# Kernel optimization log

Measured on AMD Instinct MI355X. Metric: run time of the kernel, lower is better.

Reference implementation:

```python
import jax, jax.numpy as jnp
import numpy as np

B, S, H, D = 4, 2048, 12, 64
HIDDEN = H * D  # 768
WINDOW = 64     # config.local_attention // 2
ROPE_THETA = 10000.0  # local_rope_theta for sliding layers


def rotate_half(x):
    d = x.shape[-1] // 2
    return jnp.concatenate([-x[..., d:], x[..., :d]], axis=-1)


def setup_inputs() -> dict:
    key = jax.random.key(0)
    k1, k2, k3 = jax.random.split(key, 3)
    hidden_states = jax.random.normal(k1, (B, S, HIDDEN), dtype=jnp.float32)
    # RoPE tables (HF style): inv_freq over half dims, duplicated
    inv_freq = 1.0 / (ROPE_THETA ** (jnp.arange(0, D, 2, dtype=jnp.float32) / D))  # [D/2]
    pos = jnp.arange(S, dtype=jnp.float32)
    freqs = pos[:, None] * inv_freq[None, :]          # [S, D/2]
    emb = jnp.concatenate([freqs, freqs], axis=-1)    # [S, D]
    cos = jnp.broadcast_to(jnp.cos(emb)[None], (B, S, D))
    sin = jnp.broadcast_to(jnp.sin(emb)[None], (B, S, D))
    # sliding-window additive mask [B,1,S,S]
    idx = jnp.arange(S)
    allowed = jnp.abs(idx[:, None] - idx[None, :]) <= WINDOW
    neg = jnp.finfo(jnp.float32).min
    attention_mask = jnp.broadcast_to(
        jnp.where(allowed, 0.0, neg)[None, None], (B, 1, S, S)
    ).astype(jnp.float32)
    std = 0.02
    Wqkv_w = jax.random.normal(k2, (3 * HIDDEN, HIDDEN), dtype=jnp.float32) * std
    Wo_w = jax.random.normal(k3, (HIDDEN, HIDDEN), dtype=jnp.float32) * std
    return {"hidden_states": hidden_states, "cos": cos, "sin": sin,
            "attention_mask": attention_mask, "Wqkv_w": Wqkv_w, "Wo_w": Wo_w}


def reference(hidden_states, cos, sin, attention_mask, Wqkv_w, Wo_w):
    b, s, _ = hidden_states.shape
    scaling = D ** -0.5
    qkv = hidden_states @ Wqkv_w.T                       # [B,S,3*HIDDEN]
    qkv = qkv.reshape(b, s, 3, H, D)
    q = jnp.transpose(qkv[:, :, 0], (0, 2, 1, 3))        # [B,H,S,D]
    k = jnp.transpose(qkv[:, :, 1], (0, 2, 1, 3))
    v = jnp.transpose(qkv[:, :, 2], (0, 2, 1, 3))
    # RoPE with float32 intermediates (inputs already fp32 here)
    c = cos[:, None].astype(jnp.float32)                 # [B,1,S,D]
    sn = sin[:, None].astype(jnp.float32)
    qf, kf = q.astype(jnp.float32), k.astype(jnp.float32)
    q = (qf * c + rotate_half(qf) * sn).astype(q.dtype)
    k = (kf * c + rotate_half(kf) * sn).astype(k.dtype)
    # SDPA with explicit additive mask
    scores = jnp.einsum('bhqd,bhkd->bhqk', q, k) * scaling + attention_mask
    attn = jax.nn.softmax(scores, axis=-1)
    out = jnp.einsum('bhqk,bhkd->bhqd', attn, v)         # [B,H,S,D]
    out = jnp.transpose(out, (0, 2, 1, 3)).reshape(b, s, HIDDEN)
    return out @ Wo_w.T
```

## Files before the change

kernel.cpp:

```cpp
#include <hip/hip_runtime.h>
#include <math.h>


typedef __attribute__((ext_vector_type(8))) short short8;
typedef __attribute__((ext_vector_type(4))) float floatx4;

constexpr int kB = 4;
constexpr int kS = 2048;
constexpr int kH = 12;
constexpr int kD = 64;
constexpr int kHidden = 768;
constexpr int kQKV = 3 * kHidden;

__device__ __forceinline__ unsigned short f2bf(float f) {
  union { float f; unsigned int u; } x; x.f = f;
  unsigned int r = (x.u + 0x7fffu + ((x.u >> 16) & 1u)) >> 16;
  return (unsigned short)r;
}

__global__ __launch_bounds__(256) void cvt_all(
    const float* __restrict__ h, const float* __restrict__ wqkv,
    const float* __restrict__ wo, unsigned short* __restrict__ hb,
    unsigned short* __restrict__ wqb, unsigned short* __restrict__ wob) {
  constexpr int n1 = kB * kS * kHidden / 4;
  constexpr int n2 = kQKV * kHidden / 4;
  constexpr int n3 = kHidden * kHidden / 4;
  int i = blockIdx.x * 256 + threadIdx.x;
  const float* src;
  unsigned short* dst;
  if (i < n1) {
    src = h; dst = hb;
  } else if (i < n1 + n2) {
    i -= n1; src = wqkv; dst = wqb;
  } else {
    i -= n1 + n2; if (i >= n3) return; src = wo; dst = wob;
  }
  const float4 v = ((const float4*)src)[i];
  ushort4 o;
  o.x = f2bf(v.x); o.y = f2bf(v.y); o.z = f2bf(v.z); o.w = f2bf(v.w);
  ((ushort4*)dst)[i] = o;
}

__device__ __forceinline__ void gload_lds16(const unsigned short* g, unsigned short* l) {
  __builtin_amdgcn_global_load_lds(
      (const __attribute__((address_space(1))) unsigned int*)g,
      (__attribute__((address_space(3))) unsigned int*)l, 16, 0, 0);
}

__global__ __launch_bounds__(512) void gemm_qkv(
    const unsigned short* __restrict__ A,
    const unsigned short* __restrict__ B,
    const float* __restrict__ cosp, const float* __restrict__ sinp,
    unsigned short* __restrict__ Qr, unsigned short* __restrict__ Kr,
    unsigned short* __restrict__ Vt) {
  constexpr int K = kHidden;
  constexpr int NP = 2 * (K / 64);
  __shared__ unsigned short SH[128 * 136];
  unsigned short* Ah0 = SH;
  unsigned short* Ah1 = SH + 4096;
  unsigned short* Bh0 = SH + 8192;
  unsigned short* Bh1 = SH + 12288;

  const int tid = threadIdx.x;
  const int lane = tid & 63;
  const int wave = tid >> 6;
  const int m0 = blockIdx.x * 128;
  const int n0 = blockIdx.y * 128;

  const int sc = wave * 64 + lane;
  const int srow = sc >> 2;
  const int sgc = ((sc & 3) ^ ((srow >> 1) & 3)) * 8;
  const int ldsOff = sc * 8;
  const unsigned short* gA0 = A + (size_t)(m0 + srow) * K + sgc;
  const unsigned short* gB0 = B + (size_t)(n0 + srow) * K + sgc;

  const int wm = wave >> 1, wn = wave & 1;
  const int mr = wm * 32 + (lane & 15);
  const int nr = wn * 64 + (lane & 15);
  const int kq = lane >> 4;

  int aOff[2], bOff[4];
#pragma unroll
  for (int i = 0; i < 2; i++) {
    const int r = mr + i * 16;
    aOff[i] = (r * 4 + (kq ^ ((r >> 1) & 3))) * 8;
  }
#pragma unroll
  for (int j = 0; j < 4; j++) {
    const int r = nr + j * 16;
    bOff[j] = (r * 4 + (kq ^ ((r >> 1) & 3))) * 8;
  }

  floatx4 acc[2][4];
#pragma unroll
  for (int i = 0; i < 2; i++)
#pragma unroll
    for (int j = 0; j < 4; j++) acc[i][j] = (floatx4)(0.f);

  gload_lds16(gA0, &Ah0[ldsOff]);
  gload_lds16(gB0, &Bh0[ldsOff]);

  for (int p = 0; p < NP; ++p) {
    if (p + 1 < NP) {
      const int kn = ((p + 1) >> 1) * 64 + ((p + 1) & 1) * 32;
      unsigned short* Ad = ((p + 1) & 1) ? Ah1 : Ah0;
      unsigned short* Bd = ((p + 1) & 1) ? Bh1 : Bh0;
      gload_lds16(gA0 + kn, &Ad[ldsOff]);
      gload_lds16(gB0 + kn, &Bd[ldsOff]);
      asm volatile("s_waitcnt vmcnt(2)" ::: "memory");
    } else {
      asm volatile("s_waitcnt vmcnt(0)" ::: "memory");
    }
    __builtin_amdgcn_s_barrier();
    __builtin_amdgcn_sched_barrier(0);
    const unsigned short* Asb = (p & 1) ? Ah1 : Ah0;
    const unsigned short* Bsb = (p & 1) ? Bh1 : Bh0;
    short8 af[2], bf[4];
#pragma unroll
    for (int i = 0; i < 2; i++) af[i] = *(const short8*)&Asb[aOff[i]];
#pragma unroll
    for (int j = 0; j < 4; j++) bf[j] = *(const short8*)&Bsb[bOff[j]];
#pragma unroll
    for (int i = 0; i < 2; i++)
#pragma unroll
      for (int j = 0; j < 4; j++)
        acc[i][j] = __builtin_amdgcn_mfma_f32_16x16x32_bf16(af[i], bf[j],
                                                            acc[i][j], 0, 0, 0);
    __builtin_amdgcn_sched_barrier(0);
    __builtin_amdgcn_s_barrier();
  }

  unsigned short (*Obuf)[136] = (unsigned short (*)[136])SH;

  const int region = n0 / kHidden;
  const int b = m0 >> 11, s0 = m0 & 2047;
  const int h0 = (n0 % kHidden) >> 6;
  const int rowL0 = wm * 32 + kq * 4;

  if (region == 2) {
#pragma unroll
    for (int i = 0; i < 2; i++)
#pragma unroll
      for (int r = 0; r < 4; r++) {
        const int rowL = rowL0 + i * 16 + r;
#pragma unroll
        for (int j = 0; j < 4; j++)
          Obuf[wn * 64 + j * 16 + (lane & 15)][rowL] = f2bf(acc[i][j][r]);
      }
    __syncthreads();
#pragma unroll
    for (int it = 0; it < 4; it++) {
      const int t = tid + it * 512;
      const int s8 = t & 15, rowc = t >> 4;
      const int hl = rowc >> 6, d = rowc & 63;
      *(short8*)(Vt + ((size_t)(b * kH + h0 + hl) * kD + d) * kS + s0 + s8 * 8) =
          *(const short8*)&Obuf[rowc][s8 * 8];
    }
  } else {
    unsigned short* dst = (region == 0) ? Qr : Kr;
    const float qscale = (region == 0) ? 0.125f : 1.f;
#pragma unroll
    for (int i = 0; i < 2; i++)
#pragma unroll
      for (int r = 0; r < 4; r++) {
        const int rowL = rowL0 + i * 16 + r;
        const int s = s0 + rowL;
        const float* cs = cosp + ((size_t)(b * kS + s)) * kD;
        const float* sns = sinp + ((size_t)(b * kS + s)) * kD;
#pragma unroll
        for (int jp = 0; jp < 2; jp++) {
          const int colL = wn * 64 + jp * 16 + (lane & 15);
          const int d = colL & 63;
          const float c = cs[d], sn = sns[d];
          const float xlo = acc[i][jp][r], xhi = acc[i][jp + 2][r];
          Obuf[rowL][colL]      = f2bf((xlo * c - xhi * sn) * qscale);
          Obuf[rowL][colL + 32] = f2bf((xhi * c + xlo * sn) * qscale);
        }
      }
    __syncthreads();
#pragma unroll
    for (int it = 0; it < 4; it++) {
      const int t = tid + it * 512;
      const int d8 = t & 7, sl = (t >> 3) & 127, hl = t >> 10;
      *(short8*)(dst + ((size_t)(b * kH + h0 + hl) * kS + s0 + sl) * kD + d8 * 8) =
          *(const short8*)&Obuf[sl][hl * 64 + d8 * 8];
    }
  }
}

__global__ __launch_bounds__(256) void gemm_bf16_nt(
    const unsigned short* __restrict__ A, const unsigned short* __restrict__ B,
    float* __restrict__ C, int M, int N, int K) {
  __shared__ unsigned short As[128 * 64];
  __shared__ unsigned short Bs[128 * 64];

  const int tid = threadIdx.x;
  const int lane = tid & 63;
  const int wave = tid >> 6;
  const int m0 = blockIdx.x * 128;
  const int n0 = blockIdx.y * 128;

  int ldsS[4];
  const unsigned short* gA[4];
  const unsigned short* gB[4];
#pragma unroll
  for (int t = 0; t < 4; t++) {
    const int ci = (wave * 4 + t) * 64 + lane;
    const int row = ci >> 3;
    const int c = (ci & 7) ^ (row & 7);
    ldsS[t] = ci * 8;
    gA[t] = A + (size_t)(m0 + row) * K + c * 8;
    gB[t] = B + (size_t)(n0 + row) * K + c * 8;
  }

  const int wm = wave >> 1, wn = wave & 1;
  const int mr = wm * 64 + (lane & 15);
  const int nr = wn * 64 + (lane & 15);
  const int kq = lane >> 4;

  floatx4 acc[4][4];
#pragma unroll
  for (int i = 0; i < 4; i++)
#pragma unroll
    for (int j = 0; j < 4; j++) acc[i][j] = (floatx4)(0.f);

  for (int k0 = 0; k0 < K; k0 += 64) {
    if (k0) __syncthreads();
#pragma unroll
    for (int t = 0; t < 4; t++) {
      gload_lds16(gA[t] + k0, &As[ldsS[t]]);
      gload_lds16(gB[t] + k0, &Bs[ldsS[t]]);
    }
    __syncthreads();
#pragma unroll
    for (int s = 0; s < 2; s++) {
      short8 af[4], bf[4];
#pragma unroll
      for (int i = 0; i < 4; i++) {
        af[i] = *(const short8*)&As[(mr + i * 16) * 64 + (((s * 4 + kq) ^ (mr & 7)) * 8)];
        bf[i] = *(const short8*)&Bs[(nr + i * 16) * 64 + (((s * 4 + kq) ^ (nr & 7)) * 8)];
      }
#pragma unroll
      for (int i = 0; i < 4; i++)
#pragma unroll
        for (int j = 0; j < 4; j++)
          acc[i][j] = __builtin_amdgcn_mfma_f32_16x16x32_bf16(af[i], bf[j],
                                                              acc[i][j], 0, 0, 0);
    }
  }

  const int crow = m0 + wm * 64 + kq * 4;
  const int ccol = n0 + wn * 64 + (lane & 15);
#pragma unroll
  for (int i = 0; i < 4; i++)
#pragma unroll
    for (int r = 0; r < 4; r++) {
      float* cp = C + (size_t)(crow + i * 16 + r) * N + ccol;
#pragma unroll
      for (int j = 0; j < 4; j++) cp[j * 16] = acc[i][j][r];
    }
}

constexpr int AQT = 32;

__global__ __launch_bounds__(256) void attn_v3(
    const unsigned short* __restrict__ Qr, const unsigned short* __restrict__ Kr,
    const unsigned short* __restrict__ Vt, unsigned short* __restrict__ out) {
  __shared__ unsigned short Pfrag[2][5][64][8];
  __shared__ float Ssum[2][AQT];

  const int tid = threadIdx.x;
  const int lane = tid & 63;
  const int wave = tid >> 6;
  const int quad = lane >> 4;
  const int l15 = lane & 15;
  const int qbase = blockIdx.x * AQT;
  const int h = blockIdx.y, b = blockIdx.z;
  const int bh = b * kH + h;
  const int kbase = qbase - 64;
  const int tq = wave >> 1;
  const int kh = wave & 1;

  short8 vf[2][5];
  {
    const unsigned short* vbase = Vt + (size_t)bh * kD * kS;
#pragma unroll
    for (int nt = 0; nt < 2; nt++) {
      const unsigned short* vrow = vbase + (size_t)(kh * 32 + nt * 16 + l15) * kS;
#pragma unroll
      for (int kk = 0; kk < 5; kk++) {
        int s0 = kbase + kk * 32 + quad * 8;
        s0 = min(max(s0, 0), kS - 8);
        vf[nt][kk] = *(const short8*)(vrow + s0);
      }
    }
  }

  const unsigned short* qsrc =
      Qr + ((size_t)bh * kS + qbase + tq * 16 + l15) * kD + quad * 8;
  const short8 a0 = *(const short8*)qsrc;
  const short8 a1 = *(const short8*)(qsrc + 32);

  floatx4 acc[5];
  const unsigned short* ksrc = Kr + (size_t)bh * kS * kD;
#pragma unroll
  for (int g = 0; g < 5; g++) {
    int row = kbase + (kh * 5 + g) * 16 + l15;
    row = min(max(row, 0), kS - 1);
    const unsigned short* kp = ksrc + (size_t)row * kD + quad * 8;
    const short8 b0 = *(const short8*)kp;
    const short8 b1 = *(const short8*)(kp + 32);
    floatx4 z = (floatx4)(0.f);
    z = __builtin_amdgcn_mfma_f32_16x16x32_bf16(a0, b0, z, 0, 0, 0);
    z = __builtin_amdgcn_mfma_f32_16x16x32_bf16(a1, b1, z, 0, 0, 0);
    acc[g] = z;
  }

#pragma unroll
  for (int r = 0; r < 4; r++) {
    const int q = tq * 16 + quad * 4 + r;
    float s = 0.f;
#pragma unroll
    for (int g = 0; g < 5; g++) {
      const int key = (kh * 5 + g) * 16 + l15;
      const int kg_ = kbase + key;
      const bool valid = (key >= q) && (key <= q + 128) && (kg_ >= 0) && (kg_ < kS);
      const float e = valid ? __expf(acc[g][r]) : 0.f;
      s += e;
      Pfrag[tq][key >> 5][((key >> 3) & 3) * 16 + quad * 4 + r][key & 7] = f2bf(e);
    }
#pragma unroll
    for (int off = 1; off < 16; off <<= 1) s += __shfl_xor(s, off, 64);
    if (l15 == 0) Ssum[kh][q] = s;
  }
  __syncthreads();

  floatx4 o0 = (floatx4)(0.f), o1 = (floatx4)(0.f);
#pragma unroll
  for (int kk = 0; kk < 5; kk++) {
    const short8 pa = *(const short8*)&Pfrag[tq][kk][lane][0];
    o0 = __builtin_amdgcn_mfma_f32_16x16x32_bf16(pa, vf[0][kk], o0, 0, 0, 0);
    o1 = __builtin_amdgcn_mfma_f32_16x16x32_bf16(pa, vf[1][kk], o1, 0, 0, 0);
  }

  __syncthreads();
  unsigned short (*Ob)[68] = (unsigned short (*)[68])Pfrag;
#pragma unroll
  for (int r = 0; r < 4; r++) {
    const int q = tq * 16 + quad * 4 + r;
    const float inv = 1.f / (Ssum[0][q] + Ssum[1][q]);
    Ob[q][kh * 32 + l15] = f2bf(o0[r] * inv);
    Ob[q][kh * 32 + 16 + l15] = f2bf(o1[r] * inv);
  }
  __syncthreads();
  {
    const int q = tid >> 3, d8 = tid & 7;
    *(short8*)(out + ((size_t)(b * kS + qbase + q)) * kHidden + h * kD + d8 * 8) =
        *(const short8*)&Ob[q][d8 * 8];
  }
}

extern "C" void kernel_launch(void* const* d_in, const int* in_sizes, int n_in,
                              void* d_out, int out_size, void* d_ws,
                              size_t ws_size, hipStream_t stream) {
  const float* hidden = (const float*)d_in[0];
  const float* cosp = (const float*)d_in[1];
  const float* sinp = (const float*)d_in[2];
  const float* wqkv = (const float*)d_in[4];
  const float* wo = (const float*)d_in[5];
  float* out = (float*)d_out;

  const int M = kB * kS;
  const size_t szH = (size_t)M * kHidden;

  unsigned short* hbf = (unsigned short*)d_ws;
  unsigned short* wqkvbf = hbf + szH;
  unsigned short* wobf = wqkvbf + (size_t)kQKV * kHidden;
  unsigned short* attnbf = wobf + (size_t)kHidden * kHidden;
  unsigned short* Qrb = attnbf + szH;
  unsigned short* Krb = Qrb + szH;
  unsigned short* Vtb = Krb + szH;

  const int ncvt = (M * kHidden + kQKV * kHidden + kHidden * kHidden) / 4;
  cvt_all<<<(ncvt + 255) / 256, 256, 0, stream>>>(hidden, wqkv, wo, hbf,
                                                  wqkvbf, wobf);

  dim3 g1(M / 128, kQKV / 128);
  gemm_qkv<<<g1, 512, 0, stream>>>(hbf, wqkvbf, cosp, sinp, Qrb, Krb, Vtb);

  dim3 ga(kS / AQT, kH, kB);
  attn_v3<<<ga, 256, 0, stream>>>(Qrb, Krb, Vtb, attnbf);

  dim3 g2(M / 128, kHidden / 128);
  gemm_bf16_nt<<<g2, 256, 0, stream>>>(attnbf, wobf, out, M, kHidden, kHidden);
}
```

Measured before the change: 214.7 us.

## Rebalance GEMM tiling: 4-wave QKV blocks, narrower output projection tiles

The QKV GEMM drops from 8 to 4 waves per block. Each wave now computes a 64x64 subtile with 16 accumulators instead of 32x64, which halves the LDS fragment reloads per MFMA. Each thread issues two async global-to-LDS loads per stage to keep the 128x128 tile filled. The output projection GEMM moves from 128x128 to 128x64 tiles, which doubles its grid to give more CU occupancy with a small N. The trade-off is fewer waves to hide latency in the QKV kernel and more A-tile reloads in the projection.

```diff
diff --git a/kernel.cpp b/kernel.cpp
--- a/kernel.cpp
+++ b/kernel.cpp
@@ -47,7 +47,7 @@
       (__attribute__((address_space(3))) unsigned int*)l, 16, 0, 0);
 }
 
-__global__ __launch_bounds__(512) void gemm_qkv(
+__global__ __launch_bounds__(256) void gemm_qkv(
     const unsigned short* __restrict__ A,
     const unsigned short* __restrict__ B,
     const float* __restrict__ cosp, const float* __restrict__ sinp,
@@ -64,50 +64,60 @@
   const int tid = threadIdx.x;
   const int lane = tid & 63;
   const int wave = tid >> 6;
+  const int l15 = lane & 15;
   const int m0 = blockIdx.x * 128;
   const int n0 = blockIdx.y * 128;
 
-  const int sc = wave * 64 + lane;
-  const int srow = sc >> 2;
-  const int sgc = ((sc & 3) ^ ((srow >> 1) & 3)) * 8;
-  const int ldsOff = sc * 8;
-  const unsigned short* gA0 = A + (size_t)(m0 + srow) * K + sgc;
-  const unsigned short* gB0 = B + (size_t)(n0 + srow) * K + sgc;
+  int ldsOff[2];
+  const unsigned short* gA0[2];
+  const unsigned short* gB0[2];
+#pragma unroll
+  for (int t = 0; t < 2; t++) {
+    const int sc = wave * 128 + t * 64 + lane;
+    const int srow = sc >> 2;
+    const int sgc = ((sc & 3) ^ ((srow >> 1) & 3)) * 8;
+    ldsOff[t] = sc * 8;
+    gA0[t] = A + (size_t)(m0 + srow) * K + sgc;
+    gB0[t] = B + (size_t)(n0 + srow) * K + sgc;
+  }
 
   const int wm = wave >> 1, wn = wave & 1;
-  const int mr = wm * 32 + (lane & 15);
-  const int nr = wn * 64 + (lane & 15);
+  const int mr = wm * 64 + l15;
+  const int nr = wn * 64 + l15;
   const int kq = lane >> 4;
 
-  int aOff[2], bOff[4];
-#pragma unroll
-  for (int i = 0; i < 2; i++) {
-    const int r = mr + i * 16;
-    aOff[i] = (r * 4 + (kq ^ ((r >> 1) & 3))) * 8;
-  }
-#pragma unroll
-  for (int j = 0; j < 4; j++) {
-    const int r = nr + j * 16;
-    bOff[j] = (r * 4 + (kq ^ ((r >> 1) & 3))) * 8;
-  }
-
-  floatx4 acc[2][4];
-#pragma unroll
-  for (int i = 0; i < 2; i++)
+  int aOff[4], bOff[4];
+#pragma unroll
+  for (int i = 0; i < 4; i++) {
+    const int ra = mr + i * 16;
+    aOff[i] = (ra * 4 + (kq ^ ((ra >> 1) & 3))) * 8;
+    const int rb = nr + i * 16;
+    bOff[i] = (rb * 4 + (kq ^ ((rb >> 1) & 3))) * 8;
+  }
+
+  floatx4 acc[4][4];
+#pragma unroll
+  for (int i = 0; i < 4; i++)
 #pragma unroll
     for (int j = 0; j < 4; j++) acc[i][j] = (floatx4)(0.f);
 
-  gload_lds16(gA0, &Ah0[ldsOff]);
-  gload_lds16(gB0, &Bh0[ldsOff]);
+#pragma unroll
+  for (int t = 0; t < 2; t++) {
+    gload_lds16(gA0[t], &Ah0[ldsOff[t]]);
+    gload_lds16(gB0[t], &Bh0[ldsOff[t]]);
+  }
 
   for (int p = 0; p < NP; ++p) {
     if (p + 1 < NP) {
-      const int kn = ((p + 1) >> 1) * 64 + ((p + 1) & 1) * 32;
+      const int kn = (p + 1) * 32;
       unsigned short* Ad = ((p + 1) & 1) ? Ah1 : Ah0;
       unsigned short* Bd = ((p + 1) & 1) ? Bh1 : Bh0;
-      gload_lds16(gA0 + kn, &Ad[ldsOff]);
-      gload_lds16(gB0 + kn, &Bd[ldsOff]);
-      asm volatile("s_waitcnt vmcnt(2)" ::: "memory");
+#pragma unroll
+      for (int t = 0; t < 2; t++) {
+        gload_lds16(gA0[t] + kn, &Ad[ldsOff[t]]);
+        gload_lds16(gB0[t] + kn, &Bd[ldsOff[t]]);
+      }
+      asm volatile("s_waitcnt vmcnt(4)" ::: "memory");
     } else {
       asm volatile("s_waitcnt vmcnt(0)" ::: "memory");
     }
@@ -115,13 +125,14 @@
     __builtin_amdgcn_sched_barrier(0);
     const unsigned short* Asb = (p & 1) ? Ah1 : Ah0;
     const unsigned short* Bsb = (p & 1) ? Bh1 : Bh0;
-    short8 af[2], bf[4];
-#pragma unroll
-    for (int i = 0; i < 2; i++) af[i] = *(const short8*)&Asb[aOff[i]];
-#pragma unroll
-    for (int j = 0; j < 4; j++) bf[j] = *(const short8*)&Bsb[bOff[j]];
-#pragma unroll
-    for (int i = 0; i < 2; i++)
+    short8 af[4], bf[4];
+#pragma unroll
+    for (int i = 0; i < 4; i++) {
+      af[i] = *(const short8*)&Asb[aOff[i]];
+      bf[i] = *(const short8*)&Bsb[bOff[i]];
+    }
+#pragma unroll
+    for (int i = 0; i < 4; i++)
 #pragma unroll
       for (int j = 0; j < 4; j++)
         acc[i][j] = __builtin_amdgcn_mfma_f32_16x16x32_bf16(af[i], bf[j],
@@ -135,22 +146,22 @@
   const int region = n0 / kHidden;
   const int b = m0 >> 11, s0 = m0 & 2047;
   const int h0 = (n0 % kHidden) >> 6;
-  const int rowL0 = wm * 32 + kq * 4;
+  const int rowL0 = wm * 64 + kq * 4;
 
   if (region == 2) {
 #pragma unroll
-    for (int i = 0; i < 2; i++)
+    for (int i = 0; i < 4; i++)
 #pragma unroll
       for (int r = 0; r < 4; r++) {
         const int rowL = rowL0 + i * 16 + r;
 #pragma unroll
         for (int j = 0; j < 4; j++)
-          Obuf[wn * 64 + j * 16 + (lane & 15)][rowL] = f2bf(acc[i][j][r]);
+          Obuf[wn * 64 + j * 16 + l15][rowL] = f2bf(acc[i][j][r]);
       }
     __syncthreads();
 #pragma unroll
-    for (int it = 0; it < 4; it++) {
-      const int t = tid + it * 512;
+    for (int it = 0; it < 8; it++) {
+      const int t = tid + it * 256;
       const int s8 = t & 15, rowc = t >> 4;
       const int hl = rowc >> 6, d = rowc & 63;
       *(short8*)(Vt + ((size_t)(b * kH + h0 + hl) * kD + d) * kS + s0 + s8 * 8) =
@@ -160,7 +171,7 @@
     unsigned short* dst = (region == 0) ? Qr : Kr;
     const float qscale = (region == 0) ? 0.125f : 1.f;
 #pragma unroll
-    for (int i = 0; i < 2; i++)
+    for (int i = 0; i < 4; i++)
 #pragma unroll
       for (int r = 0; r < 4; r++) {
         const int rowL = rowL0 + i * 16 + r;
@@ -169,7 +180,7 @@
         const float* sns = sinp + ((size_t)(b * kS + s)) * kD;
 #pragma unroll
         for (int jp = 0; jp < 2; jp++) {
-          const int colL = wn * 64 + jp * 16 + (lane & 15);
+          const int colL = wn * 64 + jp * 16 + l15;
           const int d = colL & 63;
           const float c = cs[d], sn = sns[d];
           const float xlo = acc[i][jp][r], xhi = acc[i][jp + 2][r];
@@ -179,8 +190,8 @@
       }
     __syncthreads();
 #pragma unroll
-    for (int it = 0; it < 4; it++) {
-      const int t = tid + it * 512;
+    for (int it = 0; it < 8; it++) {
+      const int t = tid + it * 256;
       const int d8 = t & 7, sl = (t >> 3) & 127, hl = t >> 10;
       *(short8*)(dst + ((size_t)(b * kH + h0 + hl) * kS + s0 + sl) * kD + d8 * 8) =
           *(const short8*)&Obuf[sl][hl * 64 + d8 * 8];
@@ -192,72 +203,81 @@
     const unsigned short* __restrict__ A, const unsigned short* __restrict__ B,
     float* __restrict__ C, int M, int N, int K) {
   __shared__ unsigned short As[128 * 64];
-  __shared__ unsigned short Bs[128 * 64];
+  __shared__ unsigned short Bs[64 * 64];
 
   const int tid = threadIdx.x;
   const int lane = tid & 63;
   const int wave = tid >> 6;
+  const int l15 = lane & 15;
   const int m0 = blockIdx.x * 128;
-  const int n0 = blockIdx.y * 128;
-
-  int ldsS[4];
+  const int n0 = blockIdx.y * 64;
+
+  int ldsA[4];
   const unsigned short* gA[4];
-  const unsigned short* gB[4];
 #pragma unroll
   for (int t = 0; t < 4; t++) {
     const int ci = (wave * 4 + t) * 64 + lane;
     const int row = ci >> 3;
     const int c = (ci & 7) ^ (row & 7);
-    ldsS[t] = ci * 8;
+    ldsA[t] = ci * 8;
     gA[t] = A + (size_t)(m0 + row) * K + c * 8;
+  }
+  int ldsB[2];
+  const unsigned short* gB[2];
+#pragma unroll
+  for (int t = 0; t < 2; t++) {
+    const int ci = (wave * 2 + t) * 64 + lane;
+    const int row = ci >> 3;
+    const int c = (ci & 7) ^ (row & 7);
+    ldsB[t] = ci * 8;
     gB[t] = B + (size_t)(n0 + row) * K + c * 8;
   }
 
   const int wm = wave >> 1, wn = wave & 1;
-  const int mr = wm * 64 + (lane & 15);
-  const int nr = wn * 64 + (lane & 15);
+  const int mr = wm * 64 + l15;
+  const int nr = wn * 32 + l15;
   const int kq = lane >> 4;
 
-  floatx4 acc[4][4];
+  floatx4 acc[4][2];
 #pragma unroll
   for (int i = 0; i < 4; i++)
 #pragma unroll
-    for (int j = 0; j < 4; j++) acc[i][j] = (floatx4)(0.f);
+    for (int j = 0; j < 2; j++) acc[i][j] = (floatx4)(0.f);
 
   for (int k0 = 0; k0 < K; k0 += 64) {
     if (k0) __syncthreads();
 #pragma unroll
-    for (int t = 0; t < 4; t++) {
-      gload_lds16(gA[t] + k0, &As[ldsS[t]]);
-      gload_lds16(gB[t] + k0, &Bs[ldsS[t]]);
-    }
+    for (int t = 0; t < 4; t++) gload_lds16(gA[t] + k0, &As[ldsA[t]]);
+#pragma unroll
+    for (int t = 0; t < 2; t++) gload_lds16(gB[t] + k0, &Bs[ldsB[t]]);
     __syncthreads();
 #pragma unroll
     for (int s = 0; s < 2; s++) {
-      short8 af[4], bf[4];
-#pragma unroll
-      for (int i = 0; i < 4; i++) {
-        af[i] = *(const short8*)&As[(mr + i * 16) * 64 + (((s * 4 + kq) ^ (mr & 7)) * 8)];
-        bf[i] = *(const short8*)&Bs[(nr + i * 16) * 64 + (((s * 4 + kq) ^ (nr & 7)) * 8)];
-      }
+      short8 af[4], bf[2];
 #pragma unroll
       for (int i = 0; i < 4; i++)
-#pragma unroll
-        for (int j = 0; j < 4; j++)
+        af[i] = *(const short8*)&As[(mr + i * 16) * 64 + (((s * 4 + kq) ^ ((mr + i * 16) & 7)) * 8)];
+#pragma unroll
+      for (int j = 0; j < 2; j++)
+        bf[j] = *(const short8*)&Bs[(nr + j * 16) * 64 + (((s * 4 + kq) ^ ((nr + j * 16) & 7)) * 8)];
+#pragma unroll
+      for (int i = 0; i < 4; i++)
+#pragma unroll
+        for (int j = 0; j < 2; j++)
           acc[i][j] = __builtin_amdgcn_mfma_f32_16x16x32_bf16(af[i], bf[j],
                                                               acc[i][j], 0, 0, 0);
     }
   }
 
   const int crow = m0 + wm * 64 + kq * 4;
-  const int ccol = n0 + wn * 64 + (lane & 15);
+  const int ccol = n0 + wn * 32 + l15;
 #pragma unroll
   for (int i = 0; i < 4; i++)
 #pragma unroll
     for (int r = 0; r < 4; r++) {
       float* cp = C + (size_t)(crow + i * 16 + r) * N + ccol;
 #pragma unroll
-      for (int j = 0; j < 4; j++) cp[j * 16] = acc[i][j][r];
+      for (int j = 0; j < 2; j++) cp[j * 16] = acc[i][j][r];
     }
 }
 
@@ -386,11 +406,11 @@
                                                   wqkvbf, wobf);
 
   dim3 g1(M / 128, kQKV / 128);
-  gemm_qkv<<<g1, 512, 0, stream>>>(hbf, wqkvbf, cosp, sinp, Qrb, Krb, Vtb);
+  gemm_qkv<<<g1, 256, 0, stream>>>(hbf, wqkvbf, cosp, sinp, Qrb, Krb, Vtb);
 
   dim3 ga(kS / AQT, kH, kB);
   attn_v3<<<ga, 256, 0, stream>>>(Qrb, Krb, Vtb, attnbf);
 
-  dim3 g2(M / 128, kHidden / 128);
+  dim3 g2(M / 128, kHidden / 64);
   gemm_bf16_nt<<<g2, 256, 0, stream>>>(attnbf, wobf, out, M, kHidden, kHidden);
 }
```

Result: no change. 214.7 us (+0.0%).

## Widen attention query tile to 64 and halve output GEMM N-tile

Applied to the files above, without the earlier changes.

The attention kernel now handles 64 queries per block instead of 32. Each wave computes two 16-query subtiles against six key groups, so K and V fragment loads are reused across more queries and redundant window loads drop. The output projection GEMM uses 128x64 tiles, which doubles the grid from 384 to 768 blocks so the 256 CUs are better filled. In exchange each attention block uses more registers and LDS, and the GEMM tiles have lower arithmetic intensity.

```diff
diff --git a/kernel.cpp b/kernel.cpp
--- a/kernel.cpp
+++ b/kernel.cpp
@@ -192,81 +192,90 @@
     const unsigned short* __restrict__ A, const unsigned short* __restrict__ B,
     float* __restrict__ C, int M, int N, int K) {
   __shared__ unsigned short As[128 * 64];
-  __shared__ unsigned short Bs[128 * 64];
+  __shared__ unsigned short Bs[64 * 64];
 
   const int tid = threadIdx.x;
   const int lane = tid & 63;
   const int wave = tid >> 6;
+  const int l15 = lane & 15;
   const int m0 = blockIdx.x * 128;
-  const int n0 = blockIdx.y * 128;
-
-  int ldsS[4];
+  const int n0 = blockIdx.y * 64;
+
+  int ldsA[4];
   const unsigned short* gA[4];
-  const unsigned short* gB[4];
 #pragma unroll
   for (int t = 0; t < 4; t++) {
     const int ci = (wave * 4 + t) * 64 + lane;
     const int row = ci >> 3;
     const int c = (ci & 7) ^ (row & 7);
-    ldsS[t] = ci * 8;
+    ldsA[t] = ci * 8;
     gA[t] = A + (size_t)(m0 + row) * K + c * 8;
+  }
+  int ldsB[2];
+  const unsigned short* gB[2];
+#pragma unroll
+  for (int t = 0; t < 2; t++) {
+    const int ci = (wave * 2 + t) * 64 + lane;
+    const int row = ci >> 3;
+    const int c = (ci & 7) ^ (row & 7);
+    ldsB[t] = ci * 8;
     gB[t] = B + (size_t)(n0 + row) * K + c * 8;
   }
 
   const int wm = wave >> 1, wn = wave & 1;
-  const int mr = wm * 64 + (lane & 15);
-  const int nr = wn * 64 + (lane & 15);
+  const int mr = wm * 64 + l15;
+  const int nr = wn * 32 + l15;
   const int kq = lane >> 4;
 
-  floatx4 acc[4][4];
+  floatx4 acc[4][2];
 #pragma unroll
   for (int i = 0; i < 4; i++)
 #pragma unroll
-    for (int j = 0; j < 4; j++) acc[i][j] = (floatx4)(0.f);
+    for (int j = 0; j < 2; j++) acc[i][j] = (floatx4)(0.f);
 
   for (int k0 = 0; k0 < K; k0 += 64) {
     if (k0) __syncthreads();
 #pragma unroll
-    for (int t = 0; t < 4; t++) {
-      gload_lds16(gA[t] + k0, &As[ldsS[t]]);
-      gload_lds16(gB[t] + k0, &Bs[ldsS[t]]);
-    }
+    for (int t = 0; t < 4; t++) gload_lds16(gA[t] + k0, &As[ldsA[t]]);
+#pragma unroll
+    for (int t = 0; t < 2; t++) gload_lds16(gB[t] + k0, &Bs[ldsB[t]]);
     __syncthreads();
 #pragma unroll
     for (int s = 0; s < 2; s++) {
-      short8 af[4], bf[4];
-#pragma unroll
-      for (int i = 0; i < 4; i++) {
-        af[i] = *(const short8*)&As[(mr + i * 16) * 64 + (((s * 4 + kq) ^ (mr & 7)) * 8)];
-        bf[i] = *(const short8*)&Bs[(nr + i * 16) * 64 + (((s * 4 + kq) ^ (nr & 7)) * 8)];
-      }
+      short8 af[4], bf[2];
 #pragma unroll
       for (int i = 0; i < 4; i++)
-#pragma unroll
-        for (int j = 0; j < 4; j++)
+        af[i] = *(const short8*)&As[(mr + i * 16) * 64 + (((s * 4 + kq) ^ ((mr + i * 16) & 7)) * 8)];
+#pragma unroll
+      for (int j = 0; j < 2; j++)
+        bf[j] = *(const short8*)&Bs[(nr + j * 16) * 64 + (((s * 4 + kq) ^ ((nr + j * 16) & 7)) * 8)];
+#pragma unroll
+      for (int i = 0; i < 4; i++)
+#pragma unroll
+        for (int j = 0; j < 2; j++)
           acc[i][j] = __builtin_amdgcn_mfma_f32_16x16x32_bf16(af[i], bf[j],
                                                               acc[i][j], 0, 0, 0);
     }
   }
 
   const int crow = m0 + wm * 64 + kq * 4;
-  const int ccol = n0 + wn * 64 + (lane & 15);
+  const int ccol = n0 + wn * 32 + l15;
 #pragma unroll
   for (int i = 0; i < 4; i++)
 #pragma unroll
     for (int r = 0; r < 4; r++) {
       float* cp = C + (size_t)(crow + i * 16 + r) * N + ccol;
 #pragma unroll
-      for (int j = 0; j < 4; j++) cp[j * 16] = acc[i][j][r];
-    }
-}
-
-constexpr int AQT = 32;
-
-__global__ __launch_bounds__(256) void attn_v3(
+      for (int j = 0; j < 2; j++) cp[j * 16] = acc[i][j][r];
+    }
+}
+
+constexpr int AQT = 64;
+
+__global__ __launch_bounds__(256) void attn_v4(
     const unsigned short* __restrict__ Qr, const unsigned short* __restrict__ Kr,
     const unsigned short* __restrict__ Vt, unsigned short* __restrict__ out) {
-  __shared__ unsigned short Pfrag[2][5][64][8];
+  __shared__ unsigned short Pfrag[4][6][64][8];
   __shared__ float Ssum[2][AQT];
 
   const int tid = threadIdx.x;
@@ -281,14 +290,41 @@
   const int tq = wave >> 1;
   const int kh = wave & 1;
 
-  short8 vf[2][5];
+  short8 a0[2], a1[2];
+#pragma unroll
+  for (int qs = 0; qs < 2; qs++) {
+    const unsigned short* qsrc =
+        Qr + ((size_t)bh * kS + qbase + tq * 32 + qs * 16 + l15) * kD + quad * 8;
+    a0[qs] = *(const short8*)qsrc;
+    a1[qs] = *(const short8*)(qsrc + 32);
+  }
+
+  floatx4 acc[2][6];
+  const unsigned short* ksrc = Kr + (size_t)bh * kS * kD;
+#pragma unroll
+  for (int g = 0; g < 6; g++) {
+    int row = kbase + (kh * 6 + g) * 16 + l15;
+    row = min(max(row, 0), kS - 1);
+    const unsigned short* kp = ksrc + (size_t)row * kD + quad * 8;
+    const short8 b0 = *(const short8*)kp;
+    const short8 b1 = *(const short8*)(kp + 32);
+#pragma unroll
+    for (int qs = 0; qs < 2; qs++) {
+      floatx4 z = (floatx4)(0.f);
+      z = __builtin_amdgcn_mfma_f32_16x16x32_bf16(a0[qs], b0, z, 0, 0, 0);
+      z = __builtin_amdgcn_mfma_f32_16x16x32_bf16(a1[qs], b1, z, 0, 0, 0);
+      acc[qs][g] = z;
+    }
+  }
+
+  short8 vf[2][6];
   {
     const unsigned short* vbase = Vt + (size_t)bh * kD * kS;
 #pragma unroll
     for (int nt = 0; nt < 2; nt++) {
       const unsigned short* vrow = vbase + (size_t)(kh * 32 + nt * 16 + l15) * kS;
 #pragma unroll
-      for (int kk = 0; kk < 5; kk++) {
+      for (int kk = 0; kk < 6; kk++) {
         int s0 = kbase + kk * 32 + quad * 8;
         s0 = min(max(s0, 0), kS - 8);
         vf[nt][kk] = *(const short8*)(vrow + s0);
@@ -296,65 +332,60 @@
     }
   }
 
-  const unsigned short* qsrc =
-      Qr + ((size_t)bh * kS + qbase + tq * 16 + l15) * kD + quad * 8;
-  const short8 a0 = *(const short8*)qsrc;
-  const short8 a1 = *(const short8*)(qsrc + 32);
-
-  floatx4 acc[5];
-  const unsigned short* ksrc = Kr + (size_t)bh * kS * kD;
-#pragma unroll
-  for (int g = 0; g < 5; g++) {
-    int row = kbase + (kh * 5 + g) * 16 + l15;
-    row = min(max(row, 0), kS - 1);
-    const unsigned short* kp = ksrc + (size_t)row * kD + quad * 8;
-    const short8 b0 = *(const short8*)kp;
-    const short8 b1 = *(const short8*)(kp + 32);
-    floatx4 z = (floatx4)(0.f);
-    z = __builtin_amdgcn_mfma_f32_16x16x32_bf16(a0, b0, z, 0, 0, 0);
-    z = __builtin_amdgcn_mfma_f32_16x16x32_bf16(a1, b1, z, 0, 0, 0);
-    acc[g] = z;
-  }
-
-#pragma unroll
-  for (int r = 0; r < 4; r++) {
-    const int q = tq * 16 + quad * 4 + r;
-    float s = 0.f;
-#pragma unroll
-    for (int g = 0; g < 5; g++) {
-      const int key = (kh * 5 + g) * 16 + l15;
-      const int kg_ = kbase + key;
-      const bool valid = (key >= q) && (key <= q + 128) && (kg_ >= 0) && (kg_ < kS);
-      const float e = valid ? __expf(acc[g][r]) : 0.f;
-      s += e;
-      Pfrag[tq][key >> 5][((key >> 3) & 3) * 16 + quad * 4 + r][key & 7] = f2bf(e);
-    }
-#pragma unroll
-    for (int off = 1; off < 16; off <<= 1) s += __shfl_xor(s, off, 64);
-    if (l15 == 0) Ssum[kh][q] = s;
+#pragma unroll
+  for (int qs = 0; qs < 2; qs++) {
+    const int qgrp = tq * 2 + qs;
+#pragma unroll
+    for (int r = 0; r < 4; r++) {
+      const int q = tq * 32 + qs * 16 + quad * 4 + r;
+      float s = 0.f;
+#pragma unroll
+      for (int g = 0; g < 6; g++) {
+        const int key = (kh * 6 + g) * 16 + l15;
+        const int kg_ = kbase + key;
+        const bool valid = (key >= q) && (key <= q + 128) && (kg_ >= 0) && (kg_ < kS);
+        const float e = valid ? __expf(acc[qs][g][r]) : 0.f;
+        s += e;
+        Pfrag[qgrp][key >> 5][((key >> 3) & 3) * 16 + quad * 4 + r][key & 7] = f2bf(e);
+      }
+#pragma unroll
+      for (int off = 1; off < 16; off <<= 1) s += __shfl_xor(s, off, 64);
+      if (l15 == 0) Ssum[kh][q] = s;
+    }
   }
   __syncthreads();
 
-  floatx4 o0 = (floatx4)(0.f), o1 = (floatx4)(0.f);
-#pragma unroll
-  for (int kk = 0; kk < 5; kk++) {
-    const short8 pa = *(const short8*)&Pfrag[tq][kk][lane][0];
-    o0 = __builtin_amdgcn_mfma_f32_16x16x32_bf16(pa, vf[0][kk], o0, 0, 0, 0);
-    o1 = __builtin_amdgcn_mfma_f32_16x16x32_bf16(pa, vf[1][kk], o1, 0, 0, 0);
+  floatx4 o[2][2];
+#pragma unroll
+  for (int qs = 0; qs < 2; qs++)
+#pragma unroll
+    for (int nt = 0; nt < 2; nt++) o[qs][nt] = (floatx4)(0.f);
+#pragma unroll
+  for (int kk = 0; kk < 6; kk++) {
+#pragma unroll
+    for (int qs = 0; qs < 2; qs++) {
+      const short8 pa = *(const short8*)&Pfrag[tq * 2 + qs][kk][lane][0];
+      o[qs][0] = __builtin_amdgcn_mfma_f32_16x16x32_bf16(pa, vf[0][kk], o[qs][0], 0, 0, 0);
+      o[qs][1] = __builtin_amdgcn_mfma_f32_16x16x32_bf16(pa, vf[1][kk], o[qs][1], 0, 0, 0);
+    }
   }
 
   __syncthreads();
   unsigned short (*Ob)[68] = (unsigned short (*)[68])Pfrag;
 #pragma unroll
-  for (int r = 0; r < 4; r++) {
-    const int q = tq * 16 + quad * 4 + r;
-    const float inv = 1.f / (Ssum[0][q] + Ssum[1][q]);
-    Ob[q][kh * 32 + l15] = f2bf(o0[r] * inv);
-    Ob[q][kh * 32 + 16 + l15] = f2bf(o1[r] * inv);
-  }
+  for (int qs = 0; qs < 2; qs++)
+#pragma unroll
+    for (int r = 0; r < 4; r++) {
+      const int q = tq * 32 + qs * 16 + quad * 4 + r;
+      const float inv = 1.f / (Ssum[0][q] + Ssum[1][q]);
+      Ob[q][kh * 32 + l15] = f2bf(o[qs][0][r] * inv);
+      Ob[q][kh * 32 + 16 + l15] = f2bf(o[qs][1][r] * inv);
+    }
   __syncthreads();
-  {
-    const int q = tid >> 3, d8 = tid & 7;
+#pragma unroll
+  for (int it = 0; it < 2; it++) {
+    const int t = tid + it * 256;
+    const int q = t >> 3, d8 = t & 7;
     *(short8*)(out + ((size_t)(b * kS + qbase + q)) * kHidden + h * kD + d8 * 8) =
         *(const short8*)&Ob[q][d8 * 8];
   }
@@ -389,8 +420,8 @@
   gemm_qkv<<<g1, 512, 0, stream>>>(hbf, wqkvbf, cosp, sinp, Qrb, Krb, Vtb);
 
   dim3 ga(kS / AQT, kH, kB);
-  attn_v3<<<ga, 256, 0, stream>>>(Qrb, Krb, Vtb, attnbf);
-
-  dim3 g2(M / 128, kHidden / 128);
+  attn_v4<<<ga, 256, 0, stream>>>(Qrb, Krb, Vtb, attnbf);
+
+  dim3 g2(M / 128, kHidden / 64);
   gemm_bf16_nt<<<g2, 256, 0, stream>>>(attnbf, wobf, out, M, kHidden, kHidden);
 }
```

New measurement: 206.3 us (median of 2 runs). 3.9% less time.
